# Performance work log

Measured on AMD Instinct MI355X. Metric: run time of the kernel, lower is better.

The kernel has to match this reference:

```python
import jax, jax.numpy as jnp
import numpy as np

N_NODES = 100000


def setup_inputs() -> dict:
    key = jax.random.key(0)
    k1, k2, k3 = jax.random.split(key, 3)
    x = jax.random.normal(k1, (N_NODES, 256), dtype=jnp.float32)
    edge_index = jax.random.randint(k2, (2, 1600000), 0, N_NODES, dtype=jnp.int64)
    # GCNConv learned params (glorot weight, zero bias as in PyG init)
    W = jax.random.normal(k3, (256, 64), dtype=jnp.float32) * (1.0 / np.sqrt(256.0))
    b = jnp.zeros((64,), dtype=jnp.float32)
    return {"x": x, "edge_index": edge_index, "W": W, "b": b}


def reference(x, edge_index, W, b):
    n = x.shape[0]
    # --- gcn_norm: add self-loops, symmetric normalization ---
    loops = jnp.arange(n, dtype=edge_index.dtype)
    row = jnp.concatenate([edge_index[0], loops])  # source nodes
    col = jnp.concatenate([edge_index[1], loops])  # target nodes
    ones = jnp.ones(row.shape[0], dtype=x.dtype)
    deg = jax.ops.segment_sum(ones, col, num_segments=n)  # [N]
    dinv = jnp.where(deg > 0, jax.lax.rsqrt(deg), 0.0)
    norm = dinv[row] * dinv[col]  # [E+N]
    # --- linear transform then normalized scatter-add aggregation ---
    h = x @ W  # [N, out]
    msgs = h[row] * norm[:, None]  # [E+N, out]
    out = jax.ops.segment_sum(msgs, col, num_segments=n)  # [N, out]
    return out + b
```

## Files before the change

### kernel.cpp

```cpp
#include <hip/hip_runtime.h>


#define IN_F 256
#define OUT_F 64
#define WBITS 8
#define MAXBINS 512
#define ROWMASK 0xFFFFFFu

typedef unsigned short ushort_t;
typedef short bf16x8 __attribute__((ext_vector_type(8)));
typedef float f32x4 __attribute__((ext_vector_type(4)));

static __device__ __forceinline__ unsigned f2bf1(float f) {
    unsigned u = __float_as_uint(f);
    return (u + 0x7FFFu + ((u >> 16) & 1u)) >> 16;
}
static __device__ __forceinline__ unsigned pk2(float a, float b) {
    return f2bf1(a) | (f2bf1(b) << 16);
}
static __device__ __forceinline__ ushort_t f2bf(float f) { return (ushort_t)f2bf1(f); }
static __device__ __forceinline__ float bf2f(ushort_t h) {
    return __uint_as_float(((unsigned)h) << 16);
}

__global__ __launch_bounds__(256) void bin_count_kernel(const int* __restrict__ col,
                                                        int* __restrict__ binCnt,
                                                        int E, int nbins) {
    __shared__ int hist[MAXBINS];
    int tid = threadIdx.x;
    for (int i = tid; i < nbins; i += 256) hist[i] = 0;
    __syncthreads();
    int stride = gridDim.x * 256;
    for (int e = blockIdx.x * 256 + tid; e < E; e += stride)
        atomicAdd(&hist[col[e] >> WBITS], 1);
    __syncthreads();
    for (int i = tid; i < nbins; i += 256)
        if (hist[i]) atomicAdd(&binCnt[i], hist[i]);
}

__global__ void bin_scan_kernel(const int* __restrict__ binCnt, int* __restrict__ binStart,
                                int* __restrict__ binCursor, int* __restrict__ start_n,
                                int nbins) {
    __shared__ int lds[512];
    int tid = threadIdx.x;
    int v = (tid < nbins) ? binCnt[tid] : 0;
    lds[tid] = v;
    __syncthreads();
    for (int d = 1; d < 512; d <<= 1) {
        int t = (tid >= d) ? lds[tid - d] : 0;
        __syncthreads();
        lds[tid] += t;
        __syncthreads();
    }
    if (tid < nbins) {
        int ex = lds[tid] - v;
        binStart[tid] = ex;
        binCursor[tid] = ex;
    }
    if (tid == 511) {
        binStart[nbins] = lds[511];
        start_n[0] = lds[511];
    }
}

__global__ __launch_bounds__(256) void coarse_scatter_kernel(const int* __restrict__ row,
                                                             const int* __restrict__ col,
                                                             int* __restrict__ binCursor,
                                                             unsigned* __restrict__ ebuf,
                                                             int E, int nbins) {
    __shared__ int cnt[MAXBINS];
    __shared__ int cur[MAXBINS];
    int tid = threadIdx.x;
    for (int i = tid; i < nbins; i += 256) cnt[i] = 0;
    __syncthreads();
    int chunk = (E + gridDim.x - 1) / gridDim.x;
    int s = blockIdx.x * chunk;
    int epos = min(E, s + chunk);
    for (int e = s + tid; e < epos; e += 256)
        atomicAdd(&cnt[col[e] >> WBITS], 1);
    __syncthreads();
    for (int i = tid; i < nbins; i += 256) {
        int c = cnt[i];
        cur[i] = c ? atomicAdd(&binCursor[i], c) : 0;
    }
    __syncthreads();
    for (int e = s + tid; e < epos; e += 256) {
        int cc = col[e];
        int pos = atomicAdd(&cur[cc >> WBITS], 1);
        ebuf[pos] = (unsigned)row[e] | ((unsigned)(cc & ((1 << WBITS) - 1)) << 24);
    }
}

__global__ __launch_bounds__(256) void fine_build_kernel(const unsigned* __restrict__ ebuf,
                                                         const int* __restrict__ binStart,
                                                         int* __restrict__ start,
                                                         float* __restrict__ dinv,
                                                         int* __restrict__ bucket, int n) {
    __shared__ int sdeg[256];
    __shared__ int scur[256];
    int b = blockIdx.x;
    int lo = b << WBITS;
    int wcnt = min(256, n - lo);
    int tid = threadIdx.x;
    sdeg[tid] = 0;
    __syncthreads();
    int s = binStart[b], epos = binStart[b + 1];
    for (int e = s + tid; e < epos; e += 256)
        atomicAdd(&sdeg[ebuf[e] >> 24], 1);
    __syncthreads();
    int d = sdeg[tid];
    if (tid < wcnt) dinv[lo + tid] = rsqrtf((float)(d + 1));
    for (int dd = 1; dd < 256; dd <<= 1) {
        int t = (tid >= dd) ? sdeg[tid - dd] : 0;
        __syncthreads();
        sdeg[tid] += t;
        __syncthreads();
    }
    int ex = sdeg[tid] - d;
    if (tid < wcnt) start[lo + tid] = s + ex;
    scur[tid] = ex;
    __syncthreads();
    for (int e = s + tid; e < epos; e += 256) {
        unsigned pr = ebuf[e];
        int pos = atomicAdd(&scur[pr >> 24], 1);
        bucket[s + pos] = (int)(pr & ROWMASK);
    }
}

__global__ void wfrag_kernel(const float* __restrict__ W, ushort_t* __restrict__ wfrag) {
    int t = blockIdx.x * 256 + threadIdx.x;
    if (t >= 2048) return;
    int kk = t >> 8;
    int ct = (t >> 6) & 3;
    int l  = t & 63;
    int k0 = kk * 32 + (l >> 4) * 8;
    int c  = ct * 16 + (l & 15);
    unsigned u0 = pk2(W[(k0 + 0) * OUT_F + c], W[(k0 + 1) * OUT_F + c]);
    unsigned u1 = pk2(W[(k0 + 2) * OUT_F + c], W[(k0 + 3) * OUT_F + c]);
    unsigned u2 = pk2(W[(k0 + 4) * OUT_F + c], W[(k0 + 5) * OUT_F + c]);
    unsigned u3 = pk2(W[(k0 + 6) * OUT_F + c], W[(k0 + 7) * OUT_F + c]);
    ((uint4*)wfrag)[t] = make_uint4(u0, u1, u2, u3);
}

__global__ __launch_bounds__(256) void gemm_kernel(const float* __restrict__ x,
                                                   const ushort_t* __restrict__ wfrag,
                                                   const float* __restrict__ dinv,
                                                   ushort_t* __restrict__ g, int n) {
    int tid = threadIdx.x;
    int l  = tid & 63;
    int lr = l & 15;
    int lg = l >> 4;
    int rowbase = blockIdx.x * 64 + (tid >> 6) * 16;
    int arow = rowbase + lr;
    int lrow = (arow < n) ? arow : (n - 1);
    const float* xp = x + (size_t)lrow * IN_F + lg * 8;
    const uint4* wf = (const uint4*)wfrag;

    f32x4 acc0 = {0.f, 0.f, 0.f, 0.f};
    f32x4 acc1 = {0.f, 0.f, 0.f, 0.f};
    f32x4 acc2 = {0.f, 0.f, 0.f, 0.f};
    f32x4 acc3 = {0.f, 0.f, 0.f, 0.f};

    #pragma unroll
    for (int kk = 0; kk < 8; ++kk) {
        float4 xa = *(const float4*)(xp + kk * 32);
        float4 xb = *(const float4*)(xp + kk * 32 + 4);
        union { bf16x8 v; unsigned u[4]; } A;
        A.u[0] = pk2(xa.x, xa.y);
        A.u[1] = pk2(xa.z, xa.w);
        A.u[2] = pk2(xb.x, xb.y);
        A.u[3] = pk2(xb.z, xb.w);
        union { uint4 q; bf16x8 v; } B0, B1, B2, B3;
        B0.q = wf[(kk * 4 + 0) * 64 + l];
        B1.q = wf[(kk * 4 + 1) * 64 + l];
        B2.q = wf[(kk * 4 + 2) * 64 + l];
        B3.q = wf[(kk * 4 + 3) * 64 + l];
        acc0 = __builtin_amdgcn_mfma_f32_16x16x32_bf16(A.v, B0.v, acc0, 0, 0, 0);
        acc1 = __builtin_amdgcn_mfma_f32_16x16x32_bf16(A.v, B1.v, acc1, 0, 0, 0);
        acc2 = __builtin_amdgcn_mfma_f32_16x16x32_bf16(A.v, B2.v, acc2, 0, 0, 0);
        acc3 = __builtin_amdgcn_mfma_f32_16x16x32_bf16(A.v, B3.v, acc3, 0, 0, 0);
    }

    #pragma unroll
    for (int q = 0; q < 4; ++q) {
        int r = rowbase + lg * 4 + q;
        if (r < n) {
            float dv = dinv[r];
            ushort_t* gp = g + (size_t)r * OUT_F + lr;
            gp[0]  = f2bf(acc0[q] * dv);
            gp[16] = f2bf(acc1[q] * dv);
            gp[32] = f2bf(acc2[q] * dv);
            gp[48] = f2bf(acc3[q] * dv);
        }
    }
}

__global__ __launch_bounds__(256) void gather_kernel(const int* __restrict__ start,
                              const int* __restrict__ bucket, const ushort_t* __restrict__ g,
                              const float* __restrict__ dinv, const float* __restrict__ b,
                              float* __restrict__ out, int n) {
    int lane = threadIdx.x & 63;
    int node = blockIdx.x * 4 + (threadIdx.x >> 6);
    if (node >= n) return;
    int f4  = lane & 15;
    int grp = lane >> 4;
    int s0  = start[node];
    int cnt = start[node + 1] - s0;
    const int* bp = bucket + s0;
    int last = cnt - 1;

    float4 aA = {0,0,0,0}, aB = {0,0,0,0}, aC = {0,0,0,0}, aD = {0,0,0,0};
    for (int e0 = 0; e0 < cnt; e0 += 16) {
        int eA = e0 + grp;
        int eB = e0 + 4 + grp;
        int eC = e0 + 8 + grp;
        int eD = e0 + 12 + grp;
        int iA = bp[min(eA, last)];
        int iB = bp[min(eB, last)];
        int iC = bp[min(eC, last)];
        int iD = bp[min(eD, last)];
        ushort4 vA = *(const ushort4*)(g + (size_t)iA * OUT_F + f4 * 4);
        ushort4 vB = *(const ushort4*)(g + (size_t)iB * OUT_F + f4 * 4);
        ushort4 vC = *(const ushort4*)(g + (size_t)iC * OUT_F + f4 * 4);
        ushort4 vD = *(const ushort4*)(g + (size_t)iD * OUT_F + f4 * 4);
        aA.x += (eA < cnt) ? bf2f(vA.x) : 0.f;
        aA.y += (eA < cnt) ? bf2f(vA.y) : 0.f;
        aA.z += (eA < cnt) ? bf2f(vA.z) : 0.f;
        aA.w += (eA < cnt) ? bf2f(vA.w) : 0.f;
        aB.x += (eB < cnt) ? bf2f(vB.x) : 0.f;
        aB.y += (eB < cnt) ? bf2f(vB.y) : 0.f;
        aB.z += (eB < cnt) ? bf2f(vB.z) : 0.f;
        aB.w += (eB < cnt) ? bf2f(vB.w) : 0.f;
        aC.x += (eC < cnt) ? bf2f(vC.x) : 0.f;
        aC.y += (eC < cnt) ? bf2f(vC.y) : 0.f;
        aC.z += (eC < cnt) ? bf2f(vC.z) : 0.f;
        aC.w += (eC < cnt) ? bf2f(vC.w) : 0.f;
        aD.x += (eD < cnt) ? bf2f(vD.x) : 0.f;
        aD.y += (eD < cnt) ? bf2f(vD.y) : 0.f;
        aD.z += (eD < cnt) ? bf2f(vD.z) : 0.f;
        aD.w += (eD < cnt) ? bf2f(vD.w) : 0.f;
    }
    float4 acc;
    acc.x = (aA.x + aB.x) + (aC.x + aD.x);
    acc.y = (aA.y + aB.y) + (aC.y + aD.y);
    acc.z = (aA.z + aB.z) + (aC.z + aD.z);
    acc.w = (aA.w + aB.w) + (aC.w + aD.w);
    acc.x += __shfl_xor(acc.x, 16, 64);
    acc.y += __shfl_xor(acc.y, 16, 64);
    acc.z += __shfl_xor(acc.z, 16, 64);
    acc.w += __shfl_xor(acc.w, 16, 64);
    acc.x += __shfl_xor(acc.x, 32, 64);
    acc.y += __shfl_xor(acc.y, 32, 64);
    acc.z += __shfl_xor(acc.z, 32, 64);
    acc.w += __shfl_xor(acc.w, 32, 64);

    if (grp == 0) {
        ushort4 sv = *(const ushort4*)(g + (size_t)node * OUT_F + f4 * 4);
        float dc = dinv[node];
        float4 bv = ((const float4*)b)[f4];
        float4 o;
        o.x = (acc.x + bf2f(sv.x)) * dc + bv.x;
        o.y = (acc.y + bf2f(sv.y)) * dc + bv.y;
        o.z = (acc.z + bf2f(sv.z)) * dc + bv.z;
        o.w = (acc.w + bf2f(sv.w)) * dc + bv.w;
        ((float4*)(out + (size_t)node * OUT_F))[f4] = o;
    }
}

extern "C" void kernel_launch(void* const* d_in, const int* in_sizes, int n_in,
                              void* d_out, int out_size, void* d_ws, size_t ws_size,
                              hipStream_t stream) {
    const float* x  = (const float*)d_in[0];
    const int*   ei = (const int*)d_in[1];
    const float* W  = (const float*)d_in[2];
    const float* b  = (const float*)d_in[3];
    float* out = (float*)d_out;

    int n = in_sizes[0] / IN_F;
    int E = in_sizes[1] / 2;
    const int* rowp = ei;
    const int* colp = ei + E;

    int nbins = (n + 255) >> WBITS;

    char* wp = (char*)d_ws;
    ushort_t* g   = (ushort_t*)wp;
    unsigned* ebuf = (unsigned*)wp;
    size_t r0 = (size_t)E * 4;
    size_t r1 = (size_t)n * OUT_F * 2;
    size_t roff = (r0 > r1 ? r0 : r1);
    int* bucket   = (int*)(wp + roff);
    ushort_t* wfrag = (ushort_t*)(bucket + E);
    int* start    = (int*)(wfrag + 16384);
    float* dinv   = (float*)(start + n + 1);
    int* binCnt   = (int*)(dinv + n);
    int* binStart = binCnt + MAXBINS;
    int* binCursor= binStart + MAXBINS + 1;

    wfrag_kernel<<<8, 256, 0, stream>>>(W, wfrag);
    hipMemsetAsync(binCnt, 0, MAXBINS * sizeof(int), stream);
    bin_count_kernel<<<512, 256, 0, stream>>>(colp, binCnt, E, nbins);
    bin_scan_kernel<<<1, 512, 0, stream>>>(binCnt, binStart, binCursor, start + n, nbins);
    coarse_scatter_kernel<<<512, 256, 0, stream>>>(rowp, colp, binCursor, ebuf, E, nbins);
    fine_build_kernel<<<nbins, 256, 0, stream>>>(ebuf, binStart, start, dinv, bucket, n);
    gemm_kernel<<<(n + 63) / 64, 256, 0, stream>>>(x, wfrag, dinv, g, n);
    gather_kernel<<<(n + 3) / 4, 256, 0, stream>>>(start, bucket, g, dinv, b, out, n);
}
```

Baseline: 151.9 us.

## Overlap GEMM with coarse edge scatter in one kernel and defer dinv scaling

The W-fragment packing is folded into the bin-count kernel, and the GEMM runs in the same launch as the coarse edge scatter, with separate block ranges handling each job. The memory-bound scatter and the compute-heavy GEMM can therefore run at the same time and fewer kernels are launched. Because dinv is not known while the GEMM runs, the GEMM writes unscaled h in bf16, and fine_build rescales each bin's rows by dinv afterwards in shared memory order. This adds an extra read and write of h and a second bf16 rounding. ebuf no longer aliases g, so the workspace grows.

```diff
diff --git a/kernel.cpp b/kernel.cpp
--- a/kernel.cpp
+++ b/kernel.cpp
@@ -6,6 +6,7 @@
 #define WBITS 8
 #define MAXBINS 512
 #define ROWMASK 0xFFFFFFu
+#define SCAT_BLOCKS 512
 
 typedef unsigned short ushort_t;
 typedef short bf16x8 __attribute__((ext_vector_type(8)));
@@ -23,9 +24,25 @@
     return __uint_as_float(((unsigned)h) << 16);
 }
 
-__global__ __launch_bounds__(256) void bin_count_kernel(const int* __restrict__ col,
-                                                        int* __restrict__ binCnt,
-                                                        int E, int nbins) {
+__global__ __launch_bounds__(256) void init_kernel(const float* __restrict__ W,
+                                                   ushort_t* __restrict__ wfrag,
+                                                   const int* __restrict__ col,
+                                                   int* __restrict__ binCnt,
+                                                   int E, int nbins) {
+    int gt = blockIdx.x * 256 + threadIdx.x;
+    if (gt < 2048) {
+        int t = gt;
+        int kk = t >> 8;
+        int ct = (t >> 6) & 3;
+        int l  = t & 63;
+        int k0 = kk * 32 + (l >> 4) * 8;
+        int c  = ct * 16 + (l & 15);
+        unsigned u0 = pk2(W[(k0 + 0) * OUT_F + c], W[(k0 + 1) * OUT_F + c]);
+        unsigned u1 = pk2(W[(k0 + 2) * OUT_F + c], W[(k0 + 3) * OUT_F + c]);
+        unsigned u2 = pk2(W[(k0 + 4) * OUT_F + c], W[(k0 + 5) * OUT_F + c]);
+        unsigned u3 = pk2(W[(k0 + 6) * OUT_F + c], W[(k0 + 7) * OUT_F + c]);
+        ((uint4*)wfrag)[t] = make_uint4(u0, u1, u2, u3);
+    }
     __shared__ int hist[MAXBINS];
     int tid = threadIdx.x;
     for (int i = tid; i < nbins; i += 256) hist[i] = 0;
@@ -63,31 +80,84 @@
     }
 }
 
-__global__ __launch_bounds__(256) void coarse_scatter_kernel(const int* __restrict__ row,
-                                                             const int* __restrict__ col,
-                                                             int* __restrict__ binCursor,
-                                                             unsigned* __restrict__ ebuf,
-                                                             int E, int nbins) {
+__global__ __launch_bounds__(256) void mega_kernel(const float* __restrict__ x,
+                                                   const ushort_t* __restrict__ wfrag,
+                                                   ushort_t* __restrict__ h,
+                                                   const int* __restrict__ row,
+                                                   const int* __restrict__ col,
+                                                   int* __restrict__ binCursor,
+                                                   unsigned* __restrict__ ebuf,
+                                                   int n, int E, int nbins, int gemmBlocks) {
     __shared__ int cnt[MAXBINS];
     __shared__ int cur[MAXBINS];
     int tid = threadIdx.x;
-    for (int i = tid; i < nbins; i += 256) cnt[i] = 0;
-    __syncthreads();
-    int chunk = (E + gridDim.x - 1) / gridDim.x;
-    int s = blockIdx.x * chunk;
-    int epos = min(E, s + chunk);
-    for (int e = s + tid; e < epos; e += 256)
-        atomicAdd(&cnt[col[e] >> WBITS], 1);
-    __syncthreads();
-    for (int i = tid; i < nbins; i += 256) {
-        int c = cnt[i];
-        cur[i] = c ? atomicAdd(&binCursor[i], c) : 0;
-    }
-    __syncthreads();
-    for (int e = s + tid; e < epos; e += 256) {
-        int cc = col[e];
-        int pos = atomicAdd(&cur[cc >> WBITS], 1);
-        ebuf[pos] = (unsigned)row[e] | ((unsigned)(cc & ((1 << WBITS) - 1)) << 24);
+
+    if (blockIdx.x < gemmBlocks) {
+        int l  = tid & 63;
+        int lr = l & 15;
+        int lg = l >> 4;
+        int rowbase = blockIdx.x * 64 + (tid >> 6) * 16;
+        int arow = rowbase + lr;
+        int lrow = (arow < n) ? arow : (n - 1);
+        const float* xp = x + (size_t)lrow * IN_F + lg * 8;
+        const uint4* wf = (const uint4*)wfrag;
+
+        f32x4 acc0 = {0.f, 0.f, 0.f, 0.f};
+        f32x4 acc1 = {0.f, 0.f, 0.f, 0.f};
+        f32x4 acc2 = {0.f, 0.f, 0.f, 0.f};
+        f32x4 acc3 = {0.f, 0.f, 0.f, 0.f};
+
+        #pragma unroll
+        for (int kk = 0; kk < 8; ++kk) {
+            float4 xa = *(const float4*)(xp + kk * 32);
+            float4 xb = *(const float4*)(xp + kk * 32 + 4);
+            union { bf16x8 v; unsigned u[4]; } A;
+            A.u[0] = pk2(xa.x, xa.y);
+            A.u[1] = pk2(xa.z, xa.w);
+            A.u[2] = pk2(xb.x, xb.y);
+            A.u[3] = pk2(xb.z, xb.w);
+            union { uint4 q; bf16x8 v; } B0, B1, B2, B3;
+            B0.q = wf[(kk * 4 + 0) * 64 + l];
+            B1.q = wf[(kk * 4 + 1) * 64 + l];
+            B2.q = wf[(kk * 4 + 2) * 64 + l];
+            B3.q = wf[(kk * 4 + 3) * 64 + l];
+            acc0 = __builtin_amdgcn_mfma_f32_16x16x32_bf16(A.v, B0.v, acc0, 0, 0, 0);
+            acc1 = __builtin_amdgcn_mfma_f32_16x16x32_bf16(A.v, B1.v, acc1, 0, 0, 0);
+            acc2 = __builtin_amdgcn_mfma_f32_16x16x32_bf16(A.v, B2.v, acc2, 0, 0, 0);
+            acc3 = __builtin_amdgcn_mfma_f32_16x16x32_bf16(A.v, B3.v, acc3, 0, 0, 0);
+        }
+
+        #pragma unroll
+        for (int q = 0; q < 4; ++q) {
+            int r = rowbase + lg * 4 + q;
+            if (r < n) {
+                ushort_t* gp = h + (size_t)r * OUT_F + lr;
+                gp[0]  = f2bf(acc0[q]);
+                gp[16] = f2bf(acc1[q]);
+                gp[32] = f2bf(acc2[q]);
+                gp[48] = f2bf(acc3[q]);
+            }
+        }
+    } else {
+        int sb = blockIdx.x - gemmBlocks;
+        for (int i = tid; i < nbins; i += 256) cnt[i] = 0;
+        __syncthreads();
+        int chunk = (E + SCAT_BLOCKS - 1) / SCAT_BLOCKS;
+        int s = sb * chunk;
+        int epos = min(E, s + chunk);
+        for (int e = s + tid; e < epos; e += 256)
+            atomicAdd(&cnt[col[e] >> WBITS], 1);
+        __syncthreads();
+        for (int i = tid; i < nbins; i += 256) {
+            int c = cnt[i];
+            cur[i] = c ? atomicAdd(&binCursor[i], c) : 0;
+        }
+        __syncthreads();
+        for (int e = s + tid; e < epos; e += 256) {
+            int cc = col[e];
+            int pos = atomicAdd(&cur[cc >> WBITS], 1);
+            ebuf[pos] = (unsigned)row[e] | ((unsigned)(cc & ((1 << WBITS) - 1)) << 24);
+        }
     }
 }
 
@@ -95,9 +165,11 @@
                                                          const int* __restrict__ binStart,
                                                          int* __restrict__ start,
                                                          float* __restrict__ dinv,
-                                                         int* __restrict__ bucket, int n) {
+                                                         int* __restrict__ bucket,
+                                                         ushort_t* __restrict__ g, int n) {
     __shared__ int sdeg[256];
     __shared__ int scur[256];
+    __shared__ float sdv[256];
     int b = blockIdx.x;
     int lo = b << WBITS;
     int wcnt = min(256, n - lo);
@@ -109,7 +181,9 @@
         atomicAdd(&sdeg[ebuf[e] >> 24], 1);
     __syncthreads();
     int d = sdeg[tid];
-    if (tid < wcnt) dinv[lo + tid] = rsqrtf((float)(d + 1));
+    float dv = rsqrtf((float)(d + 1));
+    sdv[tid] = dv;
+    if (tid < wcnt) dinv[lo + tid] = dv;
     for (int dd = 1; dd < 256; dd <<= 1) {
         int t = (tid >= dd) ? sdeg[tid - dd] : 0;
         __syncthreads();
@@ -125,73 +199,14 @@
         int pos = atomicAdd(&scur[pr >> 24], 1);
         bucket[s + pos] = (int)(pr & ROWMASK);
     }
-}
-
-__global__ void wfrag_kernel(const float* __restrict__ W, ushort_t* __restrict__ wfrag) {
-    int t = blockIdx.x * 256 + threadIdx.x;
-    if (t >= 2048) return;
-    int kk = t >> 8;
-    int ct = (t >> 6) & 3;
-    int l  = t & 63;
-    int k0 = kk * 32 + (l >> 4) * 8;
-    int c  = ct * 16 + (l & 15);
-    unsigned u0 = pk2(W[(k0 + 0) * OUT_F + c], W[(k0 + 1) * OUT_F + c]);
-    unsigned u1 = pk2(W[(k0 + 2) * OUT_F + c], W[(k0 + 3) * OUT_F + c]);
-    unsigned u2 = pk2(W[(k0 + 4) * OUT_F + c], W[(k0 + 5) * OUT_F + c]);
-    unsigned u3 = pk2(W[(k0 + 6) * OUT_F + c], W[(k0 + 7) * OUT_F + c]);
-    ((uint4*)wfrag)[t] = make_uint4(u0, u1, u2, u3);
-}
-
-__global__ __launch_bounds__(256) void gemm_kernel(const float* __restrict__ x,
-                                                   const ushort_t* __restrict__ wfrag,
-                                                   const float* __restrict__ dinv,
-                                                   ushort_t* __restrict__ g, int n) {
-    int tid = threadIdx.x;
-    int l  = tid & 63;
-    int lr = l & 15;
-    int lg = l >> 4;
-    int rowbase = blockIdx.x * 64 + (tid >> 6) * 16;
-    int arow = rowbase + lr;
-    int lrow = (arow < n) ? arow : (n - 1);
-    const float* xp = x + (size_t)lrow * IN_F + lg * 8;
-    const uint4* wf = (const uint4*)wfrag;
-
-    f32x4 acc0 = {0.f, 0.f, 0.f, 0.f};
-    f32x4 acc1 = {0.f, 0.f, 0.f, 0.f};
-    f32x4 acc2 = {0.f, 0.f, 0.f, 0.f};
-    f32x4 acc3 = {0.f, 0.f, 0.f, 0.f};
-
-    #pragma unroll
-    for (int kk = 0; kk < 8; ++kk) {
-        float4 xa = *(const float4*)(xp + kk * 32);
-        float4 xb = *(const float4*)(xp + kk * 32 + 4);
-        union { bf16x8 v; unsigned u[4]; } A;
-        A.u[0] = pk2(xa.x, xa.y);
-        A.u[1] = pk2(xa.z, xa.w);
-        A.u[2] = pk2(xb.x, xb.y);
-        A.u[3] = pk2(xb.z, xb.w);
-        union { uint4 q; bf16x8 v; } B0, B1, B2, B3;
-        B0.q = wf[(kk * 4 + 0) * 64 + l];
-        B1.q = wf[(kk * 4 + 1) * 64 + l];
-        B2.q = wf[(kk * 4 + 2) * 64 + l];
-        B3.q = wf[(kk * 4 + 3) * 64 + l];
-        acc0 = __builtin_amdgcn_mfma_f32_16x16x32_bf16(A.v, B0.v, acc0, 0, 0, 0);
-        acc1 = __builtin_amdgcn_mfma_f32_16x16x32_bf16(A.v, B1.v, acc1, 0, 0, 0);
-        acc2 = __builtin_amdgcn_mfma_f32_16x16x32_bf16(A.v, B2.v, acc2, 0, 0, 0);
-        acc3 = __builtin_amdgcn_mfma_f32_16x16x32_bf16(A.v, B3.v, acc3, 0, 0, 0);
-    }
-
-    #pragma unroll
-    for (int q = 0; q < 4; ++q) {
-        int r = rowbase + lg * 4 + q;
-        if (r < n) {
-            float dv = dinv[r];
-            ushort_t* gp = g + (size_t)r * OUT_F + lr;
-            gp[0]  = f2bf(acc0[q] * dv);
-            gp[16] = f2bf(acc1[q] * dv);
-            gp[32] = f2bf(acc2[q] * dv);
-            gp[48] = f2bf(acc3[q] * dv);
-        }
+    unsigned* gw = (unsigned*)(g + (size_t)lo * OUT_F);
+    int total = wcnt * 32;
+    for (int idx = tid; idx < total; idx += 256) {
+        unsigned u = gw[idx];
+        float sc = sdv[idx >> 5];
+        float a = bf2f((ushort_t)(u & 0xFFFF)) * sc;
+        float c = bf2f((ushort_t)(u >> 16)) * sc;
+        gw[idx] = pk2(a, c);
     }
 }
 
@@ -284,25 +299,24 @@
     int nbins = (n + 255) >> WBITS;
 
     char* wp = (char*)d_ws;
-    ushort_t* g   = (ushort_t*)wp;
-    unsigned* ebuf = (unsigned*)wp;
-    size_t r0 = (size_t)E * 4;
-    size_t r1 = (size_t)n * OUT_F * 2;
-    size_t roff = (r0 > r1 ? r0 : r1);
-    int* bucket   = (int*)(wp + roff);
+    ushort_t* g    = (ushort_t*)wp;
+    unsigned* ebuf = (unsigned*)(wp + (size_t)n * OUT_F * 2);
+    int* bucket    = (int*)(ebuf + E);
     ushort_t* wfrag = (ushort_t*)(bucket + E);
-    int* start    = (int*)(wfrag + 16384);
-    float* dinv   = (float*)(start + n + 1);
-    int* binCnt   = (int*)(dinv + n);
-    int* binStart = binCnt + MAXBINS;
-    int* binCursor= binStart + MAXBINS + 1;
-
-    wfrag_kernel<<<8, 256, 0, stream>>>(W, wfrag);
+    int* start     = (int*)(wfrag + 16384);
+    float* dinv    = (float*)(start + n + 1);
+    int* binCnt    = (int*)(dinv + n);
+    int* binStart  = binCnt + MAXBINS;
+    int* binCursor = binStart + MAXBINS + 1;
+
+    int gemmBlocks = (n + 63) / 64;
+
     hipMemsetAsync(binCnt, 0, MAXBINS * sizeof(int), stream);
-    bin_count_kernel<<<512, 256, 0, stream>>>(colp, binCnt, E, nbins);
+    init_kernel<<<512, 256, 0, stream>>>(W, wfrag, colp, binCnt, E, nbins);
     bin_scan_kernel<<<1, 512, 0, stream>>>(binCnt, binStart, binCursor, start + n, nbins);
-    coarse_scatter_kernel<<<512, 256, 0, stream>>>(rowp, colp, binCursor, ebuf, E, nbins);
-    fine_build_kernel<<<nbins, 256, 0, stream>>>(ebuf, binStart, start, dinv, bucket, n);
-    gemm_kernel<<<(n + 63) / 64, 256, 0, stream>>>(x, wfrag, dinv, g, n);
+    mega_kernel<<<gemmBlocks + SCAT_BLOCKS, 256, 0, stream>>>(x, wfrag, g, rowp, colp,
+                                                              binCursor, ebuf, n, E, nbins,
+                                                              gemmBlocks);
+    fine_build_kernel<<<nbins, 256, 0, stream>>>(ebuf, binStart, start, dinv, bucket, g, n);
     gather_kernel<<<(n + 3) / 4, 256, 0, stream>>>(start, bucket, g, dinv, b, out, n);
 }
```

Measured after the change: 151.6 us. No clear change (-0.2%).
